# Performance work log

Hardware: AMD Instinct MI355X
Metric: run time of the kernel (lower is better)

Reference implementation:

```python
import jax, jax.numpy as jnp
import numpy as np
from math import sqrt

DIM = 64
N_HEADS = 12
B, T = 4, 2048


def setup_inputs() -> dict:
    key = jax.random.key(0)
    ks = jax.random.split(key, 5)
    scale = 1.0 / sqrt(DIM)
    x = jax.random.normal(ks[0], (B, T, DIM), dtype=jnp.float32)
    # torch Linear(dim, h*dim) weight is (h*dim, dim); store transposed (dim, h*dim)
    Wq = jax.random.uniform(ks[1], (DIM, N_HEADS * DIM), dtype=jnp.float32, minval=-scale, maxval=scale)
    Wk = jax.random.uniform(ks[2], (DIM, N_HEADS * DIM), dtype=jnp.float32, minval=-scale, maxval=scale)
    Wv = jax.random.uniform(ks[3], (DIM, N_HEADS * DIM), dtype=jnp.float32, minval=-scale, maxval=scale)
    # finalDense: Linear(h*dim, dim) -> stored (h*dim, dim)
    Wo = jax.random.uniform(ks[4], (N_HEADS * DIM, DIM), dtype=jnp.float32,
                            minval=-1.0 / sqrt(N_HEADS * DIM), maxval=1.0 / sqrt(N_HEADS * DIM))
    return {"x": x, "Wq": Wq, "Wk": Wk, "Wv": Wv, "Wo": Wo}


def reference(x, Wq, Wk, Wv, Wo):
    b, t, k = x.shape
    h = Wq.shape[1] // k
    # NOTE: the original module does .view(b,t,h,k).view(b*h,t,k), a flat
    # row-major memory reinterpretation (NOT a head transpose). jnp.reshape
    # is the same flat reshape, so this is faithful.
    Q = (x @ Wq).reshape(b * h, t, k)
    K = (x @ Wk).reshape(b * h, t, k)
    V = (x @ Wv).reshape(b * h, t, k)
    # W[b,i,j] = sum_k K[b,i,k] * Q[b,j,k], scaled; softmax over j (last dim)
    W = jnp.einsum('bik,bjk->bij', K, Q) / sqrt(k)
    W = jax.nn.softmax(W, axis=2)
    Z = jnp.einsum('bij,bjk->bik', W, V)  # (b*h, t, k)
    Z = Z.reshape(b, t, h * k)  # flat reinterpretation, matches torch views
    return Z @ Wo
```

## Files before the change

### kernel.cpp

```cpp
#include <hip/hip_runtime.h>
#include <hip/hip_bf16.h>


#define DIM 64
#define NH 12
#define HD 768
#define BT 8192
#define TSEQ 2048
#define NSLICE 48
#define SLICE (TSEQ*DIM)

#define LDQ 72
#define LDP 72
#define LDT 72

typedef unsigned short ushort;
typedef __attribute__((ext_vector_type(8))) short bf16x8;
typedef __attribute__((ext_vector_type(4))) float f32x4;

#define SCALE2 0.18033688011112042f

__device__ __forceinline__ ushort f2b(float f) {
    union { float f; unsigned int i; } v; v.f = f;
    unsigned int x = v.i;
    return (ushort)((x + 0x7fffu + ((x >> 16) & 1u)) >> 16);
}

__global__ __launch_bounds__(256) void prep_w(
    const float* __restrict__ Wq, const float* __restrict__ Wk,
    const float* __restrict__ Wv, const float* __restrict__ Wo,
    ushort* __restrict__ Wt, ushort* __restrict__ Wot)
{
    __shared__ float tile[64][65];
    int bx = blockIdx.x;
    int z = bx / 12, bt = bx % 12;
    const float* __restrict__ IN = (z == 0) ? Wq : (z == 1) ? Wk : (z == 2) ? Wv : Wo;
    int inStride  = (z < 3) ? HD : DIM;
    int outStride = (z < 3) ? DIM : HD;
    int rbase = (z < 3) ? 0 : bt * 64;
    int cbase = (z < 3) ? bt * 64 : 0;
    ushort* __restrict__ OUT = (z < 3) ? (Wt + (size_t)z * HD * DIM) : Wot;
    int t = threadIdx.x;
    int r = t >> 2, c0 = (t & 3) * 16;
    #pragma unroll
    for (int cc = 0; cc < 16; cc += 4) {
        float4 a = *(const float4*)&IN[(size_t)(rbase + r) * inStride + cbase + c0 + cc];
        tile[r][c0 + cc] = a.x; tile[r][c0 + cc + 1] = a.y;
        tile[r][c0 + cc + 2] = a.z; tile[r][c0 + cc + 3] = a.w;
    }
    __syncthreads();
    int cl = t >> 2, r0 = (t & 3) * 16;
    ushort tmp[16] __attribute__((aligned(16)));
    #pragma unroll
    for (int rr = 0; rr < 16; ++rr) tmp[rr] = f2b(tile[r0 + rr][cl]);
    *(float4*)&OUT[(size_t)(cbase + cl) * outStride + rbase + r0] = *(const float4*)tmp;
    *(float4*)&OUT[(size_t)(cbase + cl) * outStride + rbase + r0 + 8] = *(const float4*)&tmp[8];
}

__global__ __launch_bounds__(256) void qkv_kernel(
    const float* __restrict__ x, const ushort* __restrict__ Wt,
    ushort* __restrict__ Q, ushort* __restrict__ K, ushort* __restrict__ V)
{
    int rt = blockIdx.x, half = blockIdx.y;
    int t = threadIdx.x, w = t >> 6, lane = t & 63;
    int ln = lane & 15, q = lane >> 4;
    int m0 = rt * 64 + w * 16;

    float4 xa = *(const float4*)&x[(size_t)(m0 + ln) * DIM + q * 8];
    float4 xb_ = *(const float4*)&x[(size_t)(m0 + ln) * DIM + q * 8 + 4];
    float4 xc = *(const float4*)&x[(size_t)(m0 + ln) * DIM + 32 + q * 8];
    float4 xd = *(const float4*)&x[(size_t)(m0 + ln) * DIM + 32 + q * 8 + 4];
    ushort ta[8] __attribute__((aligned(16)));
    ushort tb[8] __attribute__((aligned(16)));
    ta[0]=f2b(xa.x); ta[1]=f2b(xa.y); ta[2]=f2b(xa.z); ta[3]=f2b(xa.w);
    ta[4]=f2b(xb_.x); ta[5]=f2b(xb_.y); ta[6]=f2b(xb_.z); ta[7]=f2b(xb_.w);
    tb[0]=f2b(xc.x); tb[1]=f2b(xc.y); tb[2]=f2b(xc.z); tb[3]=f2b(xc.w);
    tb[4]=f2b(xd.x); tb[5]=f2b(xd.y); tb[6]=f2b(xd.z); tb[7]=f2b(xd.w);
    bf16x8 af0 = *(const bf16x8*)ta;
    bf16x8 af1 = *(const bf16x8*)tb;

    for (int cc = 0; cc < 18; ++cc) {
        int ct = half * 18 + cc;
        int which = ct / 12;
        int col0 = (ct % 12) * 64;
        const ushort* __restrict__ Wz = Wt + (size_t)which * HD * DIM;
        ushort* __restrict__ Y = (which == 0) ? Q : (which == 1) ? K : V;
        float sc = (which == 0) ? SCALE2 : 1.f;
        #pragma unroll
        for (int nt = 0; nt < 4; ++nt) {
            int n = col0 + nt * 16 + ln;
            bf16x8 bf0 = *(const bf16x8*)&Wz[(size_t)n * DIM + q * 8];
            bf16x8 bf1 = *(const bf16x8*)&Wz[(size_t)n * DIM + 32 + q * 8];
            f32x4 acc = (f32x4){0.f, 0.f, 0.f, 0.f};
            acc = __builtin_amdgcn_mfma_f32_16x16x32_bf16(af0, bf0, acc, 0, 0, 0);
            acc = __builtin_amdgcn_mfma_f32_16x16x32_bf16(af1, bf1, acc, 0, 0, 0);
            #pragma unroll
            for (int r = 0; r < 4; ++r)
                Y[(size_t)(m0 + q * 4 + r) * HD + col0 + nt * 16 + ln] = f2b(acc[r] * sc);
        }
    }
}

__global__ __launch_bounds__(256) void vtrans_kernel(
    const ushort* __restrict__ V, ushort* __restrict__ Vt)
{
    __shared__ ushort tileT[64 * LDT];
    int tt = blockIdx.x, s = blockIdx.y;
    const ushort* __restrict__ Vp = V + (size_t)s * SLICE;
    ushort* __restrict__ Vo = Vt + (size_t)s * SLICE;
    int t = threadIdx.x;
    int r = t >> 3, c = (t & 7) * 8;
    ushort va[8] __attribute__((aligned(16)));
    ushort vb[8] __attribute__((aligned(16)));
    *(float4*)va = *(const float4*)&Vp[(size_t)(tt * 64 + r) * DIM + c];
    *(float4*)vb = *(const float4*)&Vp[(size_t)(tt * 64 + r + 32) * DIM + c];
    int g0 = ((r >> 3) ^ (c >> 3)) * 8 + (r & 7);
    int g1 = (((r + 32) >> 3) ^ (c >> 3)) * 8 + (r & 7);
    #pragma unroll
    for (int k = 0; k < 8; ++k) {
        tileT[(c + k) * LDT + g0] = va[k];
        tileT[(c + k) * LDT + g1] = vb[k];
    }
    __syncthreads();
    #pragma unroll
    for (int j = 0; j < 2; ++j) {
        int flat = t + 256 * j;
        int d = flat >> 3, tg = flat & 7;
        int sg = tg ^ ((d >> 3) & 7);
        float4 vv = *(const float4*)&tileT[d * LDT + sg * 8];
        *(float4*)&Vo[(size_t)d * TSEQ + tt * 64 + tg * 8] = vv;
    }
}

__global__ __launch_bounds__(256) void attn_kernel(
    const ushort* __restrict__ Qs, const ushort* __restrict__ Ks,
    const ushort* __restrict__ Vts, ushort* __restrict__ Zs)
{
    __shared__ ushort Qt[64 * LDQ];
    __shared__ ushort Vtile[64 * LDQ];
    __shared__ ushort Pw[128 * LDP];
    int itile = blockIdx.x, s = blockIdx.y;
    const ushort* __restrict__ Qp = Qs + (size_t)s * SLICE;
    const ushort* __restrict__ Kp = Ks + (size_t)s * SLICE;
    const ushort* __restrict__ Vp = Vts + (size_t)s * SLICE;
    ushort* __restrict__ Zp = Zs + (size_t)s * SLICE;
    int t = threadIdx.x, w = t >> 6, lane = t & 63;
    int ln = lane & 15, q = lane >> 4;

    bf16x8 kf[2][2];
    #pragma unroll
    for (int ih = 0; ih < 2; ++ih) {
        int i0 = itile * 128 + w * 32 + ih * 16 + ln;
        kf[ih][0] = *(const bf16x8*)&Kp[(size_t)i0 * DIM + q * 8];
        kf[ih][1] = *(const bf16x8*)&Kp[(size_t)i0 * DIM + 32 + q * 8];
    }
    f32x4 Of[2][4];
    #pragma unroll
    for (int ih = 0; ih < 2; ++ih)
        #pragma unroll
        for (int dt = 0; dt < 4; ++dt) Of[ih][dt] = (f32x4){0.f, 0.f, 0.f, 0.f};
    float lsum[2] = {0.f, 0.f};
    ushort* Pme = &Pw[w * 32 * LDP];

    int sr = t >> 3, sc = (t & 7) * 8;
    float4 qa0 = *(const float4*)&Qp[(size_t)sr * DIM + sc];
    float4 qa1 = *(const float4*)&Qp[(size_t)(sr + 32) * DIM + sc];
    float4 va0 = *(const float4*)&Vp[(size_t)sr * TSEQ + sc];
    float4 va1 = *(const float4*)&Vp[(size_t)(sr + 32) * TSEQ + sc];

    for (int jt = 0; jt < TSEQ; jt += 64) {
        __syncthreads();
        *(float4*)&Qt[sr * LDQ + sc] = qa0;
        *(float4*)&Qt[(sr + 32) * LDQ + sc] = qa1;
        *(float4*)&Vtile[sr * LDQ + sc] = va0;
        *(float4*)&Vtile[(sr + 32) * LDQ + sc] = va1;
        __syncthreads();
        if (jt + 64 < TSEQ) {
            qa0 = *(const float4*)&Qp[(size_t)(jt + 64 + sr) * DIM + sc];
            qa1 = *(const float4*)&Qp[(size_t)(jt + 64 + sr + 32) * DIM + sc];
            va0 = *(const float4*)&Vp[(size_t)sr * TSEQ + jt + 64 + sc];
            va1 = *(const float4*)&Vp[(size_t)(sr + 32) * TSEQ + jt + 64 + sc];
        }

        f32x4 Sf[2][4];
        #pragma unroll
        for (int mt = 0; mt < 4; ++mt) {
            bf16x8 a0 = *(const bf16x8*)&Qt[(mt * 16 + ln) * LDQ + q * 8];
            bf16x8 a1 = *(const bf16x8*)&Qt[(mt * 16 + ln) * LDQ + 32 + q * 8];
            #pragma unroll
            for (int ih = 0; ih < 2; ++ih) {
                f32x4 acc = (f32x4){0.f, 0.f, 0.f, 0.f};
                acc = __builtin_amdgcn_mfma_f32_16x16x32_bf16(a0, kf[ih][0], acc, 0, 0, 0);
                acc = __builtin_amdgcn_mfma_f32_16x16x32_bf16(a1, kf[ih][1], acc, 0, 0, 0);
                Sf[ih][mt] = acc;
            }
        }
        #pragma unroll
        for (int ih = 0; ih < 2; ++ih) {
            float ls = 0.f;
            #pragma unroll
            for (int mt = 0; mt < 4; ++mt) {
                float p0 = __builtin_amdgcn_exp2f(Sf[ih][mt][0]);
                float p1 = __builtin_amdgcn_exp2f(Sf[ih][mt][1]);
                float p2 = __builtin_amdgcn_exp2f(Sf[ih][mt][2]);
                float p3 = __builtin_amdgcn_exp2f(Sf[ih][mt][3]);
                unsigned int b0 = __float_as_uint(p0), b1 = __float_as_uint(p1);
                unsigned int b2 = __float_as_uint(p2), b3 = __float_as_uint(p3);
                unsigned int t1 = b1 & 0xFFFF0000u, t3 = b3 & 0xFFFF0000u;
                unsigned int h01 = (b0 >> 16) | t1;
                unsigned int h23 = (b2 >> 16) | t3;
                ls += __uint_as_float(h01 << 16) + __uint_as_float(t1)
                    + __uint_as_float(h23 << 16) + __uint_as_float(t3);
                *(uint2*)&Pme[(ih * 16 + ln) * LDP + mt * 16 + q * 4] =
                    make_uint2(h01, h23);
            }
            lsum[ih] += ls;
        }
        bf16x8 pa[2][2];
        #pragma unroll
        for (int ih = 0; ih < 2; ++ih) {
            pa[ih][0] = *(const bf16x8*)&Pme[(ih * 16 + ln) * LDP + q * 8];
            pa[ih][1] = *(const bf16x8*)&Pme[(ih * 16 + ln) * LDP + 32 + q * 8];
        }
        #pragma unroll
        for (int dt = 0; dt < 4; ++dt) {
            bf16x8 vb0 = *(const bf16x8*)&Vtile[(dt * 16 + ln) * LDQ + q * 8];
            bf16x8 vb1 = *(const bf16x8*)&Vtile[(dt * 16 + ln) * LDQ + 32 + q * 8];
            #pragma unroll
            for (int ih = 0; ih < 2; ++ih) {
                Of[ih][dt] = __builtin_amdgcn_mfma_f32_16x16x32_bf16(pa[ih][0], vb0, Of[ih][dt], 0, 0, 0);
                Of[ih][dt] = __builtin_amdgcn_mfma_f32_16x16x32_bf16(pa[ih][1], vb1, Of[ih][dt], 0, 0, 0);
            }
        }
    }
    float linv_r[2][4];
    #pragma unroll
    for (int ih = 0; ih < 2; ++ih) {
        float l = lsum[ih];
        l += __shfl_xor(l, 16);
        l += __shfl_xor(l, 32);
        float linv = 1.f / l;
        #pragma unroll
        for (int r = 0; r < 4; ++r) linv_r[ih][r] = __shfl(linv, q * 4 + r);
    }
    #pragma unroll
    for (int ih = 0; ih < 2; ++ih)
        #pragma unroll
        for (int dt = 0; dt < 4; ++dt)
            #pragma unroll
            for (int r = 0; r < 4; ++r)
                Pme[(ih * 16 + q * 4 + r) * LDP + dt * 16 + ln] =
                    f2b(Of[ih][dt][r] * linv_r[ih][r]);
    __syncthreads();
    int zr = t >> 1, zc = (t & 1) * 32;
    size_t zoff = (size_t)(itile * 128 + zr) * DIM + zc;
    #pragma unroll
    for (int c4 = 0; c4 < 4; ++c4)
        *(float4*)&Zp[zoff + c4 * 8] = *(const float4*)&Pw[zr * LDP + zc + c4 * 8];
}

__global__ __launch_bounds__(64) void out_kernel(
    const ushort* __restrict__ Z, const ushort* __restrict__ Wot,
    float* __restrict__ out)
{
    int m0 = blockIdx.x * 32;
    int lane = threadIdx.x;
    int ln = lane & 15, q = lane >> 4;
    f32x4 acc[2][4];
    #pragma unroll
    for (int u = 0; u < 2; ++u)
        #pragma unroll
        for (int nt = 0; nt < 4; ++nt) acc[u][nt] = (f32x4){0.f, 0.f, 0.f, 0.f};
    for (int kc = 0; kc < 24; ++kc) {
        bf16x8 a0 = *(const bf16x8*)&Z[(size_t)(m0 + ln) * HD + kc * 32 + q * 8];
        bf16x8 a1 = *(const bf16x8*)&Z[(size_t)(m0 + 16 + ln) * HD + kc * 32 + q * 8];
        #pragma unroll
        for (int nt = 0; nt < 4; ++nt) {
            bf16x8 bf = *(const bf16x8*)&Wot[(size_t)(nt * 16 + ln) * HD + kc * 32 + q * 8];
            acc[0][nt] = __builtin_amdgcn_mfma_f32_16x16x32_bf16(a0, bf, acc[0][nt], 0, 0, 0);
            acc[1][nt] = __builtin_amdgcn_mfma_f32_16x16x32_bf16(a1, bf, acc[1][nt], 0, 0, 0);
        }
    }
    #pragma unroll
    for (int u = 0; u < 2; ++u)
        #pragma unroll
        for (int nt = 0; nt < 4; ++nt)
            #pragma unroll
            for (int r = 0; r < 4; ++r)
                out[(size_t)(m0 + u * 16 + q * 4 + r) * DIM + nt * 16 + ln] = acc[u][nt][r];
}

extern "C" void kernel_launch(void* const* d_in, const int* in_sizes, int n_in,
                              void* d_out, int out_size, void* d_ws, size_t ws_size,
                              hipStream_t stream)
{
    const float* x  = (const float*)d_in[0];
    const float* Wq = (const float*)d_in[1];
    const float* Wk = (const float*)d_in[2];
    const float* Wv = (const float*)d_in[3];
    const float* Wo = (const float*)d_in[4];
    float* out = (float*)d_out;

    const size_t n = (size_t)BT * HD;
    ushort* Q   = (ushort*)d_ws;
    ushort* K   = Q + n;
    ushort* V   = K + n;
    ushort* Vt  = V + n;
    ushort* Wt  = Vt;
    ushort* Wot = Vt + n;
    ushort* Z   = V;

    prep_w<<<48, 256, 0, stream>>>(Wq, Wk, Wv, Wo, Wt, Wot);
    qkv_kernel<<<dim3(128, 2), 256, 0, stream>>>(x, Wt, Q, K, V);
    vtrans_kernel<<<dim3(32, 48), 256, 0, stream>>>(V, Vt);
    attn_kernel<<<dim3(16, 48), 256, 0, stream>>>(Q, K, Vt, Z);
    out_kernel<<<256, 64, 0, stream>>>(Z, Wot, out);
}
```

Measured before the change: 180.5 us.

## Split attention key dimension across waves, read Q/V directly, reduce via LDS atomics

Restructures the attention kernel so each block handles 64 query rows and its four waves split the 2048-long summed dimension, each wave loading its own Q and V fragments straight from global memory into registers. This removes the per-iteration shared-memory staging and both block barriers inside the loop. Partial outputs and row sums are then combined with LDS float atomics before normalisation. The grid is flattened to 1536 blocks with an XCD-aware mapping so that blocks sharing a slice run on the same XCD for L2 reuse. In exchange it adds atomic reduction cost, higher register pressure (16 accumulator tiles), and uncoalesced direct global loads.

```diff
diff --git a/kernel.cpp b/kernel.cpp
--- a/kernel.cpp
+++ b/kernel.cpp
@@ -136,74 +136,62 @@
     const ushort* __restrict__ Qs, const ushort* __restrict__ Ks,
     const ushort* __restrict__ Vts, ushort* __restrict__ Zs)
 {
-    __shared__ ushort Qt[64 * LDQ];
-    __shared__ ushort Vtile[64 * LDQ];
-    __shared__ ushort Pw[128 * LDP];
-    int itile = blockIdx.x, s = blockIdx.y;
-    const ushort* __restrict__ Qp = Qs + (size_t)s * SLICE;
-    const ushort* __restrict__ Kp = Ks + (size_t)s * SLICE;
-    const ushort* __restrict__ Vp = Vts + (size_t)s * SLICE;
-    ushort* __restrict__ Zp = Zs + (size_t)s * SLICE;
+    __shared__ ushort Pw[4][64 * LDP];
+    __shared__ float Ored[64][68];
+    __shared__ float Ls[64];
+    int bid = blockIdx.x;
+    int xcd = bid & 7, rest = bid >> 3;
+    int slice = xcd * 6 + (rest >> 5);
+    int itile = rest & 31;
+    const ushort* __restrict__ Qp = Qs + (size_t)slice * SLICE;
+    const ushort* __restrict__ Kp = Ks + (size_t)slice * SLICE;
+    const ushort* __restrict__ Vp = Vts + (size_t)slice * SLICE;
+    ushort* __restrict__ Zp = Zs + (size_t)slice * SLICE;
     int t = threadIdx.x, w = t >> 6, lane = t & 63;
     int ln = lane & 15, q = lane >> 4;
-
-    bf16x8 kf[2][2];
-    #pragma unroll
-    for (int ih = 0; ih < 2; ++ih) {
-        int i0 = itile * 128 + w * 32 + ih * 16 + ln;
+    ushort* Pme = &Pw[w][0];
+
+    bf16x8 kf[4][2];
+    #pragma unroll
+    for (int ih = 0; ih < 4; ++ih) {
+        int i0 = itile * 64 + ih * 16 + ln;
         kf[ih][0] = *(const bf16x8*)&Kp[(size_t)i0 * DIM + q * 8];
         kf[ih][1] = *(const bf16x8*)&Kp[(size_t)i0 * DIM + 32 + q * 8];
     }
-    f32x4 Of[2][4];
-    #pragma unroll
-    for (int ih = 0; ih < 2; ++ih)
+    f32x4 Of[4][4];
+    #pragma unroll
+    for (int ih = 0; ih < 4; ++ih)
         #pragma unroll
         for (int dt = 0; dt < 4; ++dt) Of[ih][dt] = (f32x4){0.f, 0.f, 0.f, 0.f};
-    float lsum[2] = {0.f, 0.f};
-    ushort* Pme = &Pw[w * 32 * LDP];
-
-    int sr = t >> 3, sc = (t & 7) * 8;
-    float4 qa0 = *(const float4*)&Qp[(size_t)sr * DIM + sc];
-    float4 qa1 = *(const float4*)&Qp[(size_t)(sr + 32) * DIM + sc];
-    float4 va0 = *(const float4*)&Vp[(size_t)sr * TSEQ + sc];
-    float4 va1 = *(const float4*)&Vp[(size_t)(sr + 32) * TSEQ + sc];
-
-    for (int jt = 0; jt < TSEQ; jt += 64) {
-        __syncthreads();
-        *(float4*)&Qt[sr * LDQ + sc] = qa0;
-        *(float4*)&Qt[(sr + 32) * LDQ + sc] = qa1;
-        *(float4*)&Vtile[sr * LDQ + sc] = va0;
-        *(float4*)&Vtile[(sr + 32) * LDQ + sc] = va1;
-        __syncthreads();
-        if (jt + 64 < TSEQ) {
-            qa0 = *(const float4*)&Qp[(size_t)(jt + 64 + sr) * DIM + sc];
-            qa1 = *(const float4*)&Qp[(size_t)(jt + 64 + sr + 32) * DIM + sc];
-            va0 = *(const float4*)&Vp[(size_t)sr * TSEQ + jt + 64 + sc];
-            va1 = *(const float4*)&Vp[(size_t)(sr + 32) * TSEQ + jt + 64 + sc];
-        }
-
-        f32x4 Sf[2][4];
-        #pragma unroll
-        for (int mt = 0; mt < 4; ++mt) {
-            bf16x8 a0 = *(const bf16x8*)&Qt[(mt * 16 + ln) * LDQ + q * 8];
-            bf16x8 a1 = *(const bf16x8*)&Qt[(mt * 16 + ln) * LDQ + 32 + q * 8];
-            #pragma unroll
-            for (int ih = 0; ih < 2; ++ih) {
+    float lsum[4] = {0.f, 0.f, 0.f, 0.f};
+
+    bf16x8 aq[4][2];
+    #pragma unroll
+    for (int mt = 0; mt < 4; ++mt) {
+        int jr = w * 64 + mt * 16 + ln;
+        aq[mt][0] = *(const bf16x8*)&Qp[(size_t)jr * DIM + q * 8];
+        aq[mt][1] = *(const bf16x8*)&Qp[(size_t)jr * DIM + 32 + q * 8];
+    }
+
+    for (int jt = 0; jt < TSEQ; jt += 256) {
+        int jw = jt + w * 64;
+        #pragma unroll
+        for (int ih = 0; ih < 4; ++ih) {
+            f32x4 Sf[4];
+            #pragma unroll
+            for (int mt = 0; mt < 4; ++mt) {
                 f32x4 acc = (f32x4){0.f, 0.f, 0.f, 0.f};
-                acc = __builtin_amdgcn_mfma_f32_16x16x32_bf16(a0, kf[ih][0], acc, 0, 0, 0);
-                acc = __builtin_amdgcn_mfma_f32_16x16x32_bf16(a1, kf[ih][1], acc, 0, 0, 0);
-                Sf[ih][mt] = acc;
+                acc = __builtin_amdgcn_mfma_f32_16x16x32_bf16(aq[mt][0], kf[ih][0], acc, 0, 0, 0);
+                acc = __builtin_amdgcn_mfma_f32_16x16x32_bf16(aq[mt][1], kf[ih][1], acc, 0, 0, 0);
+                Sf[mt] = acc;
             }
-        }
-        #pragma unroll
-        for (int ih = 0; ih < 2; ++ih) {
             float ls = 0.f;
             #pragma unroll
             for (int mt = 0; mt < 4; ++mt) {
-                float p0 = __builtin_amdgcn_exp2f(Sf[ih][mt][0]);
-                float p1 = __builtin_amdgcn_exp2f(Sf[ih][mt][1]);
-                float p2 = __builtin_amdgcn_exp2f(Sf[ih][mt][2]);
-                float p3 = __builtin_amdgcn_exp2f(Sf[ih][mt][3]);
+                float p0 = __builtin_amdgcn_exp2f(Sf[mt][0]);
+                float p1 = __builtin_amdgcn_exp2f(Sf[mt][1]);
+                float p2 = __builtin_amdgcn_exp2f(Sf[mt][2]);
+                float p3 = __builtin_amdgcn_exp2f(Sf[mt][3]);
                 unsigned int b0 = __float_as_uint(p0), b1 = __float_as_uint(p1);
                 unsigned int b2 = __float_as_uint(p2), b3 = __float_as_uint(p3);
                 unsigned int t1 = b1 & 0xFFFF0000u, t3 = b3 & 0xFFFF0000u;
@@ -216,47 +204,65 @@
             }
             lsum[ih] += ls;
         }
-        bf16x8 pa[2][2];
-        #pragma unroll
-        for (int ih = 0; ih < 2; ++ih) {
+        if (jt + 256 < TSEQ) {
+            #pragma unroll
+            for (int mt = 0; mt < 4; ++mt) {
+                int jr = jt + 256 + w * 64 + mt * 16 + ln;
+                aq[mt][0] = *(const bf16x8*)&Qp[(size_t)jr * DIM + q * 8];
+                aq[mt][1] = *(const bf16x8*)&Qp[(size_t)jr * DIM + 32 + q * 8];
+            }
+        }
+        bf16x8 vb[4][2];
+        #pragma unroll
+        for (int dt = 0; dt < 4; ++dt) {
+            vb[dt][0] = *(const bf16x8*)&Vp[(size_t)(dt * 16 + ln) * TSEQ + jw + q * 8];
+            vb[dt][1] = *(const bf16x8*)&Vp[(size_t)(dt * 16 + ln) * TSEQ + jw + 32 + q * 8];
+        }
+        bf16x8 pa[4][2];
+        #pragma unroll
+        for (int ih = 0; ih < 4; ++ih) {
             pa[ih][0] = *(const bf16x8*)&Pme[(ih * 16 + ln) * LDP + q * 8];
             pa[ih][1] = *(const bf16x8*)&Pme[(ih * 16 + ln) * LDP + 32 + q * 8];
         }
         #pragma unroll
-        for (int dt = 0; dt < 4; ++dt) {
-            bf16x8 vb0 = *(const bf16x8*)&Vtile[(dt * 16 + ln) * LDQ + q * 8];
-            bf16x8 vb1 = *(const bf16x8*)&Vtile[(dt * 16 + ln) * LDQ + 32 + q * 8];
-            #pragma unroll
-            for (int ih = 0; ih < 2; ++ih) {
-                Of[ih][dt] = __builtin_amdgcn_mfma_f32_16x16x32_bf16(pa[ih][0], vb0, Of[ih][dt], 0, 0, 0);
-                Of[ih][dt] = __builtin_amdgcn_mfma_f32_16x16x32_bf16(pa[ih][1], vb1, Of[ih][dt], 0, 0, 0);
+        for (int dt = 0; dt < 4; ++dt)
+            #pragma unroll
+            for (int ih = 0; ih < 4; ++ih) {
+                Of[ih][dt] = __builtin_amdgcn_mfma_f32_16x16x32_bf16(pa[ih][0], vb[dt][0], Of[ih][dt], 0, 0, 0);
+                Of[ih][dt] = __builtin_amdgcn_mfma_f32_16x16x32_bf16(pa[ih][1], vb[dt][1], Of[ih][dt], 0, 0, 0);
             }
-        }
-    }
-    float linv_r[2][4];
-    #pragma unroll
-    for (int ih = 0; ih < 2; ++ih) {
+    }
+
+    #pragma unroll
+    for (int ih = 0; ih < 4; ++ih) {
         float l = lsum[ih];
         l += __shfl_xor(l, 16);
         l += __shfl_xor(l, 32);
-        float linv = 1.f / l;
-        #pragma unroll
-        for (int r = 0; r < 4; ++r) linv_r[ih][r] = __shfl(linv, q * 4 + r);
-    }
-    #pragma unroll
-    for (int ih = 0; ih < 2; ++ih)
+        lsum[ih] = l;
+    }
+    __syncthreads();
+    for (int k = t; k < 64 * 68; k += 256) (&Ored[0][0])[k] = 0.f;
+    if (t < 64) Ls[t] = 0.f;
+    __syncthreads();
+    #pragma unroll
+    for (int ih = 0; ih < 4; ++ih)
+        if (q == 0) atomicAdd(&Ls[ih * 16 + ln], lsum[ih]);
+    #pragma unroll
+    for (int ih = 0; ih < 4; ++ih)
         #pragma unroll
         for (int dt = 0; dt < 4; ++dt)
             #pragma unroll
             for (int r = 0; r < 4; ++r)
-                Pme[(ih * 16 + q * 4 + r) * LDP + dt * 16 + ln] =
-                    f2b(Of[ih][dt][r] * linv_r[ih][r]);
-    __syncthreads();
-    int zr = t >> 1, zc = (t & 1) * 32;
-    size_t zoff = (size_t)(itile * 128 + zr) * DIM + zc;
-    #pragma unroll
-    for (int c4 = 0; c4 < 4; ++c4)
-        *(float4*)&Zp[zoff + c4 * 8] = *(const float4*)&Pw[zr * LDP + zc + c4 * 8];
+                atomicAdd(&Ored[ih * 16 + q * 4 + r][dt * 16 + ln], Of[ih][dt][r]);
+    __syncthreads();
+    int i = t >> 2, d0 = (t & 3) * 16;
+    float linv = 1.f / Ls[i];
+    ushort tmp[16] __attribute__((aligned(16)));
+    #pragma unroll
+    for (int k = 0; k < 16; ++k) tmp[k] = f2b(Ored[i][d0 + k] * linv);
+    size_t zoff = (size_t)(itile * 64 + i) * DIM + d0;
+    *(float4*)&Zp[zoff] = *(const float4*)tmp;
+    *(float4*)&Zp[zoff + 8] = *(const float4*)&tmp[8];
 }
 
 __global__ __launch_bounds__(64) void out_kernel(
@@ -313,6 +319,6 @@
     prep_w<<<48, 256, 0, stream>>>(Wq, Wk, Wv, Wo, Wt, Wot);
     qkv_kernel<<<dim3(128, 2), 256, 0, stream>>>(x, Wt, Q, K, V);
     vtrans_kernel<<<dim3(32, 48), 256, 0, stream>>>(V, Vt);
-    attn_kernel<<<dim3(16, 48), 256, 0, stream>>>(Q, K, Vt, Z);
+    attn_kernel<<<1536, 256, 0, stream>>>(Q, K, Vt, Z);
     out_kernel<<<256, 64, 0, stream>>>(Z, Wot, out);
 }
```

Result: slower. 333.4 us (+84.7%).
